# Kernel tuning notes

Hardware: AMD Instinct MI355X
Metric: run time of the kernel (lower is better)

Reference implementation:

```python
import jax, jax.numpy as jnp
import numpy as np

K = 7        # kernel_dim
P = 3        # padding
G = 1        # groups
EPS = 1e-5   # BatchNorm eps


def _unfold(X):
    # X: (B, C, H, W) -> patches (B, C, K*K, H, W), torch.nn.Unfold ordering (C major, then kh, kw)
    B, C, H, W = X.shape
    Xp = jnp.pad(X, ((0, 0), (0, 0), (P, P), (P, P)))
    pats = [Xp[:, :, i:i + H, j:j + W] for i in range(K) for j in range(K)]
    return jnp.stack(pats, axis=2)


def setup_inputs() -> dict:
    key = jax.random.key(0)
    ks = jax.random.split(key, 4)
    B, C, H, W = 2, 64, 128, 128
    Cr = 16  # out_dim // reduction
    return {
        "X": jax.random.normal(ks[0], (B, C, H, W), dtype=jnp.float32),
        "w_reduce": jax.random.normal(ks[1], (Cr, C), dtype=jnp.float32) * 0.05,
        "b_reduce": jnp.zeros((Cr,), dtype=jnp.float32),
        "gamma": jnp.ones((Cr,), dtype=jnp.float32),
        "beta": jnp.zeros((Cr,), dtype=jnp.float32),
        "w_span": jax.random.normal(ks[2], (K * K * G, Cr), dtype=jnp.float32) * 0.05,
        "b_span": jnp.zeros((K * K * G,), dtype=jnp.float32),
    }


def reference(X, w_reduce, b_reduce, gamma, beta, w_span, b_span):
    B, C, H, W = X.shape
    out_dim = C  # in_dim == out_dim -> initial_mapping is Identity

    # unfold (im2col): (B, G, out_dim//G, K*K, H, W)
    unfolded = _unfold(X).reshape(B, G, out_dim // G, K * K, H, W)

    # kernel generation: stride==1 -> pool is Identity
    reduced = jnp.einsum('bchw,oc->bohw', X, w_reduce) + b_reduce[None, :, None, None]
    # BatchNorm2d (training mode: batch statistics) + ReLU
    mean = reduced.mean(axis=(0, 2, 3))
    var = reduced.var(axis=(0, 2, 3))
    bn = (reduced - mean[None, :, None, None]) * jax.lax.rsqrt(var + EPS)[None, :, None, None]
    act = jax.nn.relu(bn * gamma[None, :, None, None] + beta[None, :, None, None])

    kernel = jnp.einsum('bchw,kc->bkhw', act, w_span) + b_span[None, :, None, None]
    kernel = kernel.reshape(B, G, K * K, H, W)[:, :, None]  # (B, G, 1, K*K, H, W)

    out = (kernel * unfolded).sum(axis=3)  # (B, G, out_dim//G, H, W)
    return out.reshape(B, out_dim, H, W)
```

## Files before the change

### kernel.cpp

```cpp
#include <hip/hip_runtime.h>
#include <math.h>

constexpr int B  = 2, C = 64, H = 128, W = 128;
constexpr int Cr = 16;
constexpr int K  = 7, KK = 49;
constexpr int HW  = H * W;
constexpr int CHW = C * HW;
constexpr int NPIX = B * HW;
constexpr float EPS = 1e-5f;

constexpr int R_F = NPIX * Cr;
constexpr int P_F = 512 * 32;
constexpr size_t WS_NEED = (size_t)(R_F + P_F + 64) * 4;

typedef _Float16 half4v __attribute__((ext_vector_type(4)));


__global__ __launch_bounds__(256) void k_reduce_r(
    const float* __restrict__ X, const float* __restrict__ w_reduce,
    const float* __restrict__ b_reduce, float* __restrict__ r_ws,
    float* __restrict__ partial)
{
    __shared__ float wrS[Cr * C];
    __shared__ float tmpA[4][Cr][64];
    const int t = threadIdx.x;
    for (int i = t; i < Cr * C; i += 256) wrS[i] = w_reduce[i];
    __syncthreads();

    const int pixl = t & 63, cg = t >> 6;
    const int p = blockIdx.x * 64 + pixl;
    const int b = p >> 14, hw = p & (HW - 1);
    const float* xb = X + (size_t)b * CHW + hw;

    float x[16];
    #pragma unroll
    for (int i = 0; i < 16; ++i) x[i] = xb[(cg * 16 + i) * HW];

    float rp[16];
    #pragma unroll
    for (int o = 0; o < 16; ++o) rp[o] = (cg == 0) ? b_reduce[o] : 0.f;
    #pragma unroll
    for (int i = 0; i < 16; ++i) {
        const float xv = x[i];
        #pragma unroll
        for (int o = 0; o < 16; ++o)
            rp[o] = fmaf(xv, wrS[o * 64 + cg * 16 + i], rp[o]);
    }
    #pragma unroll
    for (int o = 0; o < 16; ++o) tmpA[cg][o][pixl] = rp[o];
    __syncthreads();

    float rr[4];
    #pragma unroll
    for (int j = 0; j < 4; ++j) {
        const int o = cg * 4 + j;
        rr[j] = tmpA[0][o][pixl] + tmpA[1][o][pixl] + tmpA[2][o][pixl] + tmpA[3][o][pixl];
    }
    *(float4*)&r_ws[(size_t)p * 16 + cg * 4] = make_float4(rr[0], rr[1], rr[2], rr[3]);

    float s[4], q[4];
    #pragma unroll
    for (int j = 0; j < 4; ++j) { s[j] = rr[j]; q[j] = rr[j] * rr[j]; }
    #pragma unroll
    for (int off = 32; off > 0; off >>= 1) {
        #pragma unroll
        for (int j = 0; j < 4; ++j) {
            s[j] += __shfl_down(s[j], off);
            q[j] += __shfl_down(q[j], off);
        }
    }
    if ((t & 63) == 0) {
        #pragma unroll
        for (int j = 0; j < 4; ++j) {
            partial[blockIdx.x * 32 + cg * 4 + j]      = s[j];
            partial[blockIdx.x * 32 + 16 + cg * 4 + j] = q[j];
        }
    }
}

constexpr int TLH = 8, TLW = 16;
constexpr int HR = TLH + 6, HC = TLW + 6;
constexpr int RPT6 = 24;
constexpr int CSP6 = HR * RPT6;

__global__ __launch_bounds__(256) void k_inv6(
    const float* __restrict__ X, const float* __restrict__ r_ws,
    const float* __restrict__ partial, const float* __restrict__ gamma,
    const float* __restrict__ beta, const float* __restrict__ w_span,
    const float* __restrict__ b_span, float* __restrict__ out)
{
    __shared__ _Float16 Xs[32 * CSP6];
    __shared__ _Float16 kcS[KK * 128];
    __shared__ float wspS[KK * Cr];
    __shared__ float bspS[KK + 3];
    __shared__ float red[256];
    __shared__ float scS[16], ofS[16];

    const int t   = threadIdx.x;
    const int raw = blockIdx.x;
    const int wg  = (raw & 7) * 64 + (raw >> 3);
    const int tile = wg & 127;
    const int half = (wg >> 7) & 1;
    const int b    = wg >> 8;
    const int th0 = (tile >> 3) * TLH;
    const int tw0 = (tile & 7) * TLW;

    const int px = t & 127;
    const int kh2 = t >> 7;
    const int p1r = px >> 4, p1c = px & 15;
    const size_t gp = (size_t)b * HW + (size_t)(th0 + p1r) * W + (tw0 + p1c);
    const float4 r0 = *(const float4*)&r_ws[gp * 16 + 0];
    const float4 r1 = *(const float4*)&r_ws[gp * 16 + 4];
    const float4 r2 = *(const float4*)&r_ws[gp * 16 + 8];
    const float4 r3 = *(const float4*)&r_ws[gp * 16 + 12];

    {
        const int scol = t & 31;
        const int sch  = t >> 5;
        const int gw   = tw0 + scol - 3;
        const bool wok = (unsigned)gw < (unsigned)W;
        const float* xg = X + (size_t)b * CHW + (size_t)(half * 32) * HW;
        #pragma unroll
        for (int cb = 0; cb < 4; ++cb) {
            const int c = cb * 8 + sch;
            const float* xc = xg + (size_t)c * HW;
            _Float16* xs = Xs + c * CSP6 + scol;
            #pragma unroll
            for (int r = 0; r < HR; ++r) {
                const int gh = th0 + r - 3;
                float v = 0.f;
                if (wok && (unsigned)gh < (unsigned)H) v = xc[gh * W + gw];
                if (scol < HC) xs[r * RPT6] = (_Float16)v;
            }
        }
    }

    if (t < 196) *(float4*)&wspS[t * 4] = *(const float4*)&w_span[t * 4];
    if (t >= 196 && t < 196 + KK) bspS[t - 196] = b_span[t - 196];

    {
        const int o = t & 31, seg = t >> 5;
        float acc = 0.f;
        #pragma unroll 16
        for (int j = 0; j < 64; ++j) acc += partial[(size_t)(seg * 64 + j) * 32 + o];
        red[seg * 32 + o] = acc;
    }
    __syncthreads();
    if (t < 64) {
        const int o2 = t & 31;
        float tot = 0.f;
        #pragma unroll
        for (int g = 0; g < 8; ++g) tot += red[g * 32 + o2];
        const float sq = __shfl(tot, (t & 31) + 16);
        if (t < 16) {
            const float mean = tot / (float)NPIX;
            const float var  = sq / (float)NPIX - mean * mean;
            const float sc   = gamma[t] * rsqrtf(var + EPS);
            scS[t] = sc;
            ofS[t] = beta[t] - mean * sc;
        }
    }
    __syncthreads();

    {
        float act[16];
        const float rv[16] = {r0.x, r0.y, r0.z, r0.w, r1.x, r1.y, r1.z, r1.w,
                              r2.x, r2.y, r2.z, r2.w, r3.x, r3.y, r3.z, r3.w};
        #pragma unroll
        for (int o = 0; o < 16; ++o)
            act[o] = fmaxf(fmaf(scS[o], rv[o], ofS[o]), 0.f);
        #pragma unroll
        for (int j = 0; j < 25; ++j) {
            const int k = kh2 * 25 + j;
            if (k < KK) {
                const float4 w0 = *(const float4*)&wspS[k * 16 + 0];
                const float4 w1 = *(const float4*)&wspS[k * 16 + 4];
                const float4 w2 = *(const float4*)&wspS[k * 16 + 8];
                const float4 w3 = *(const float4*)&wspS[k * 16 + 12];
                float v = bspS[k];
                v = fmaf(act[0],  w0.x, v); v = fmaf(act[1],  w0.y, v);
                v = fmaf(act[2],  w0.z, v); v = fmaf(act[3],  w0.w, v);
                v = fmaf(act[4],  w1.x, v); v = fmaf(act[5],  w1.y, v);
                v = fmaf(act[6],  w1.z, v); v = fmaf(act[7],  w1.w, v);
                v = fmaf(act[8],  w2.x, v); v = fmaf(act[9],  w2.y, v);
                v = fmaf(act[10], w2.z, v); v = fmaf(act[11], w2.w, v);
                v = fmaf(act[12], w3.x, v); v = fmaf(act[13], w3.y, v);
                v = fmaf(act[14], w3.z, v); v = fmaf(act[15], w3.w, v);
                kcS[k * 128 + px] = (_Float16)v;
            }
        }
    }
    __syncthreads();

    const int strip = t & 31;
    const int chg   = t >> 5;
    const int pr3 = strip >> 2, pc = (strip & 3) * 4;
    const int c0  = chg * 4;

    float acc[4][4];
    #pragma unroll
    for (int i = 0; i < 4; ++i)
        #pragma unroll
        for (int j = 0; j < 4; ++j) acc[i][j] = 0.f;

    #pragma unroll
    for (int kh = 0; kh < 7; ++kh) {
        half4v kcr[7];
        #pragma unroll
        for (int kw = 0; kw < 7; ++kw)
            kcr[kw] = *(const half4v*)&kcS[(kh * 7 + kw) * 128 + pr3 * 16 + pc];
        #pragma unroll
        for (int i = 0; i < 4; ++i) {
            const _Float16* xr = &Xs[(c0 + i) * CSP6 + (pr3 + kh) * RPT6 + pc];
            const half4v xa = *(const half4v*)&xr[0];
            const half4v xb = *(const half4v*)&xr[4];
            const half4v xc = *(const half4v*)&xr[8];
            const _Float16 xw[12] = {xa[0], xa[1], xa[2], xa[3],
                                     xb[0], xb[1], xb[2], xb[3],
                                     xc[0], xc[1], xc[2], xc[3]};
            #pragma unroll
            for (int kw = 0; kw < 7; ++kw)
                #pragma unroll
                for (int j = 0; j < 4; ++j)
                    acc[i][j] = fmaf((float)kcr[kw][j], (float)xw[kw + j], acc[i][j]);
        }
    }

    float* ob = out + (size_t)b * CHW + (size_t)(half * 32 + c0) * HW
                    + (size_t)(th0 + pr3) * W + (tw0 + pc);
    #pragma unroll
    for (int i = 0; i < 4; ++i)
        *(float4*)&ob[(size_t)i * HW] = make_float4(acc[i][0], acc[i][1], acc[i][2], acc[i][3]);
}


constexpr int XS_F  = C * 196;
constexpr int KC_F  = KK * 64;
constexpr int ACT_F = Cr * 64;
constexpr int WR_F  = Cr * C;
constexpr int WSP_F = KK * Cr;
constexpr int SMEM_F = XS_F + KC_F + ACT_F + WR_F + WSP_F + KK + Cr + Cr;
constexpr int SMEM_BYTES = SMEM_F * 4;

__global__ __launch_bounds__(128) void k_reduce_stats(
    const float* __restrict__ X, const float* __restrict__ w_reduce,
    const float* __restrict__ b_reduce, float* __restrict__ partial)
{
    __shared__ float wr[WR_F];
    __shared__ float brd[Cr];
    __shared__ float tmp[2][32];
    const int t = threadIdx.x;
    for (int i = t; i < WR_F; i += 128) wr[i] = w_reduce[i];
    if (t < Cr) brd[t] = b_reduce[t];
    __syncthreads();
    const int p  = blockIdx.x * 128 + t;
    const int b  = p >> 14;
    const int hw = p & (HW - 1);
    const float* xb = X + b * CHW + hw;
    float r[Cr];
    #pragma unroll
    for (int o = 0; o < Cr; ++o) r[o] = brd[o];
    #pragma unroll 4
    for (int c = 0; c < C; ++c) {
        const float x = xb[c * HW];
        #pragma unroll
        for (int o = 0; o < Cr; ++o) r[o] = fmaf(x, wr[o * C + c], r[o]);
    }
    const int lane = t & 63, wv = t >> 6;
    #pragma unroll
    for (int o = 0; o < Cr; ++o) {
        float s = r[o], q = r[o] * r[o];
        #pragma unroll
        for (int off = 32; off > 0; off >>= 1) {
            s += __shfl_down(s, off);
            q += __shfl_down(q, off);
        }
        if (lane == 0) { tmp[wv][o] = s; tmp[wv][Cr + o] = q; }
    }
    __syncthreads();
    if (t < 32) partial[blockIdx.x * 32 + t] = tmp[0][t] + tmp[1][t];
}

__global__ __launch_bounds__(256) void k_stats_final(
    const float* __restrict__ partial, float* __restrict__ stats)
{
    __shared__ float red[256];
    __shared__ float fin[32];
    const int t = threadIdx.x;
    const int o = t & 31, g = t >> 5;
    float acc = 0.f;
    #pragma unroll 8
    for (int j = 0; j < 32; ++j) acc += partial[(g * 32 + j) * 32 + o];
    red[t] = acc;
    __syncthreads();
    if (t < 32) {
        float v = 0.f;
        #pragma unroll
        for (int g2 = 0; g2 < 8; ++g2) v += red[g2 * 32 + t];
        fin[t] = v;
    }
    __syncthreads();
    if (t < Cr) {
        const float mean = fin[t] / (float)NPIX;
        const float var  = fin[Cr + t] / (float)NPIX - mean * mean;
        stats[t]      = mean;
        stats[Cr + t] = rsqrtf(var + EPS);
    }
}

__global__ __launch_bounds__(256) void k_involution(
    const float* __restrict__ X, const float* __restrict__ w_reduce,
    const float* __restrict__ b_reduce, const float* __restrict__ gamma,
    const float* __restrict__ beta, const float* __restrict__ w_span,
    const float* __restrict__ b_span, const float* __restrict__ stats,
    float* __restrict__ out)
{
    extern __shared__ float smem[];
    float* Xs   = smem;
    float* kcS  = Xs  + XS_F;
    float* actS = kcS + KC_F;
    float* wrS  = actS + ACT_F;
    float* wspS = wrS + WR_F;
    float* bspS = wspS + WSP_F;
    float* scS  = bspS + KK;
    float* ofS  = scS + Cr;
    const int t    = threadIdx.x;
    const int bx   = blockIdx.x;
    const int b    = bx >> 8;
    const int tile = bx & 255;
    const int h0   = (tile >> 4) << 3;
    const int w0   = (tile & 15) << 3;
    const float* xbg = X + b * CHW;
    for (int idx = t; idx < XS_F; idx += 256) {
        const int c   = idx / 196;
        const int rem = idx - c * 196;
        const int r   = rem / 14;
        const int col = rem - r * 14;
        const int gh  = h0 + r - 3, gw = w0 + col - 3;
        float v = 0.f;
        if ((unsigned)gh < (unsigned)H && (unsigned)gw < (unsigned)W)
            v = xbg[c * HW + gh * W + gw];
        Xs[idx] = v;
    }
    for (int i = t; i < WR_F;  i += 256) wrS[i]  = w_reduce[i];
    for (int i = t; i < WSP_F; i += 256) wspS[i] = w_span[i];
    if (t < KK) bspS[t] = b_span[t];
    if (t < Cr) {
        const float m  = stats[t];
        const float rs = stats[Cr + t];
        const float gm = gamma[t];
        scS[t] = gm * rs;
        ofS[t] = (b_reduce[t] - m) * gm * rs + beta[t];
    }
    __syncthreads();
    const int pix = t & 63;
    const int grp = t >> 6;
    const int ph  = pix >> 3, pw = pix & 7;
    {
        const int base = (ph + 3) * 14 + (pw + 3);
        float d0 = 0.f, d1 = 0.f, d2 = 0.f, d3 = 0.f;
        #pragma unroll 8
        for (int c = 0; c < C; ++c) {
            const float x = Xs[c * 196 + base];
            d0 = fmaf(x, wrS[(grp * 4 + 0) * C + c], d0);
            d1 = fmaf(x, wrS[(grp * 4 + 1) * C + c], d1);
            d2 = fmaf(x, wrS[(grp * 4 + 2) * C + c], d2);
            d3 = fmaf(x, wrS[(grp * 4 + 3) * C + c], d3);
        }
        const float d[4] = {d0, d1, d2, d3};
        #pragma unroll
        for (int j = 0; j < 4; ++j) {
            const int o = grp * 4 + j;
            actS[o * 64 + pix] = fmaxf(fmaf(scS[o], d[j], ofS[o]), 0.f);
        }
    }
    __syncthreads();
    for (int k = grp; k < KK; k += 4) {
        float v = bspS[k];
        #pragma unroll
        for (int o = 0; o < Cr; ++o)
            v = fmaf(actS[o * 64 + pix], wspS[k * Cr + o], v);
        kcS[k * 64 + pix] = v;
    }
    __syncthreads();
    float acc[16];
    #pragma unroll
    for (int i = 0; i < 16; ++i) acc[i] = 0.f;
    const float* xsc = Xs + grp * 16 * 196;
    #pragma unroll
    for (int k = 0; k < KK; ++k) {
        const int kh = k / 7, kw = k - (k / 7) * 7;
        const float kcv = kcS[k * 64 + pix];
        const int xoff = (ph + kh) * 14 + (pw + kw);
        #pragma unroll
        for (int i = 0; i < 16; ++i)
            acc[i] = fmaf(kcv, xsc[i * 196 + xoff], acc[i]);
    }
    float* ob = out + b * CHW + (grp * 16) * HW + (h0 + ph) * W + (w0 + pw);
    #pragma unroll
    for (int i = 0; i < 16; ++i) ob[i * HW] = acc[i];
}


extern "C" void kernel_launch(void* const* d_in, const int* in_sizes, int n_in,
                              void* d_out, int out_size, void* d_ws, size_t ws_size,
                              hipStream_t stream) {
    const float* X        = (const float*)d_in[0];
    const float* w_reduce = (const float*)d_in[1];
    const float* b_reduce = (const float*)d_in[2];
    const float* gamma    = (const float*)d_in[3];
    const float* beta     = (const float*)d_in[4];
    const float* w_span   = (const float*)d_in[5];
    const float* b_span   = (const float*)d_in[6];
    float* out = (float*)d_out;
    float* ws  = (float*)d_ws;

    if (ws_size >= WS_NEED) {
        float* r_ws    = ws;
        float* partial = ws + R_F;
        k_reduce_r<<<512, 256, 0, stream>>>(X, w_reduce, b_reduce, r_ws, partial);
        k_inv6<<<512, 256, 0, stream>>>(X, r_ws, partial, gamma, beta,
                                        w_span, b_span, out);
    } else {
        float* partial = ws;
        float* stats   = ws + 8192;
        hipFuncSetAttribute((const void*)k_involution,
                            hipFuncAttributeMaxDynamicSharedMemorySize, SMEM_BYTES);
        k_reduce_stats<<<256, 128, 0, stream>>>(X, w_reduce, b_reduce, partial);
        k_stats_final<<<1, 256, 0, stream>>>(partial, stats);
        k_involution<<<512, 256, SMEM_BYTES, stream>>>(
            X, w_reduce, b_reduce, gamma, beta, w_span, b_span, stats, out);
    }
}
```

Baseline: 28.96 us.

## Split reduce kernel across more blocks and transpose BN partial sums layout

The 1x1 reduce kernel now uses 32 pixels per block with 8 channel groups, launching 1024 blocks instead of 512 to expose more parallelism and memory-level concurrency. BatchNorm partial sums are stored transposed (channel-major, 1024 entries each) so the consumer kernel can read them with coalesced float4 loads instead of strided scalar loads. The trade-off is more partials to reduce per block in the main kernel and a larger shared-memory cross-group reduction.

```diff
diff --git a/kernel.cpp b/kernel.cpp
--- a/kernel.cpp
+++ b/kernel.cpp
@@ -9,72 +9,72 @@
 constexpr int NPIX = B * HW;
 constexpr float EPS = 1e-5f;
 
-constexpr int R_F = NPIX * Cr;
-constexpr int P_F = 512 * 32;
-constexpr size_t WS_NEED = (size_t)(R_F + P_F + 64) * 4;
+constexpr int R_F  = NPIX * Cr;
+constexpr int PT_F = 32 * 1024;
+constexpr size_t WS_NEED = (size_t)(R_F + PT_F + 64) * 4;
 
 typedef _Float16 half4v __attribute__((ext_vector_type(4)));
 
 
-__global__ __launch_bounds__(256) void k_reduce_r(
+__global__ __launch_bounds__(256) void k_reduce_r2(
     const float* __restrict__ X, const float* __restrict__ w_reduce,
     const float* __restrict__ b_reduce, float* __restrict__ r_ws,
-    float* __restrict__ partial)
+    float* __restrict__ partialT)
 {
     __shared__ float wrS[Cr * C];
-    __shared__ float tmpA[4][Cr][64];
+    __shared__ float brd[Cr];
+    __shared__ float tmpA[8][Cr][32];
     const int t = threadIdx.x;
-    for (int i = t; i < Cr * C; i += 256) wrS[i] = w_reduce[i];
-    __syncthreads();
-
-    const int pixl = t & 63, cg = t >> 6;
-    const int p = blockIdx.x * 64 + pixl;
+    #pragma unroll
+    for (int i = 0; i < 4; ++i) wrS[t + i * 256] = w_reduce[t + i * 256];
+    if (t < Cr) brd[t] = b_reduce[t];
+    __syncthreads();
+
+    const int pixl = t & 31, cg = t >> 5;
+    const int p = blockIdx.x * 32 + pixl;
     const int b = p >> 14, hw = p & (HW - 1);
     const float* xb = X + (size_t)b * CHW + hw;
 
-    float x[16];
-    #pragma unroll
-    for (int i = 0; i < 16; ++i) x[i] = xb[(cg * 16 + i) * HW];
+    float x[8];
+    #pragma unroll
+    for (int i = 0; i < 8; ++i) x[i] = xb[(cg * 8 + i) * HW];
 
     float rp[16];
     #pragma unroll
-    for (int o = 0; o < 16; ++o) rp[o] = (cg == 0) ? b_reduce[o] : 0.f;
-    #pragma unroll
-    for (int i = 0; i < 16; ++i) {
+    for (int o = 0; o < 16; ++o) rp[o] = 0.f;
+    #pragma unroll
+    for (int i = 0; i < 8; ++i) {
         const float xv = x[i];
         #pragma unroll
         for (int o = 0; o < 16; ++o)
-            rp[o] = fmaf(xv, wrS[o * 64 + cg * 16 + i], rp[o]);
+            rp[o] = fmaf(xv, wrS[o * 64 + cg * 8 + i], rp[o]);
     }
     #pragma unroll
     for (int o = 0; o < 16; ++o) tmpA[cg][o][pixl] = rp[o];
     __syncthreads();
 
-    float rr[4];
-    #pragma unroll
-    for (int j = 0; j < 4; ++j) {
-        const int o = cg * 4 + j;
-        rr[j] = tmpA[0][o][pixl] + tmpA[1][o][pixl] + tmpA[2][o][pixl] + tmpA[3][o][pixl];
-    }
-    *(float4*)&r_ws[(size_t)p * 16 + cg * 4] = make_float4(rr[0], rr[1], rr[2], rr[3]);
-
-    float s[4], q[4];
-    #pragma unroll
-    for (int j = 0; j < 4; ++j) { s[j] = rr[j]; q[j] = rr[j] * rr[j]; }
-    #pragma unroll
-    for (int off = 32; off > 0; off >>= 1) {
-        #pragma unroll
-        for (int j = 0; j < 4; ++j) {
-            s[j] += __shfl_down(s[j], off);
-            q[j] += __shfl_down(q[j], off);
-        }
-    }
-    if ((t & 63) == 0) {
-        #pragma unroll
-        for (int j = 0; j < 4; ++j) {
-            partial[blockIdx.x * 32 + cg * 4 + j]      = s[j];
-            partial[blockIdx.x * 32 + 16 + cg * 4 + j] = q[j];
-        }
+    const int o0 = cg * 2;
+    float r0 = brd[o0], r1 = brd[o0 + 1];
+    #pragma unroll
+    for (int g = 0; g < 8; ++g) {
+        r0 += tmpA[g][o0][pixl];
+        r1 += tmpA[g][o0 + 1][pixl];
+    }
+    *(float2*)&r_ws[(size_t)p * 16 + o0] = make_float2(r0, r1);
+
+    float s0 = r0, q0 = r0 * r0, s1 = r1, q1 = r1 * r1;
+    #pragma unroll
+    for (int off = 16; off > 0; off >>= 1) {
+        s0 += __shfl_down(s0, off);
+        q0 += __shfl_down(q0, off);
+        s1 += __shfl_down(s1, off);
+        q1 += __shfl_down(q1, off);
+    }
+    if (pixl == 0) {
+        partialT[(size_t)o0 * 1024 + blockIdx.x]            = s0;
+        partialT[(size_t)(o0 + 1) * 1024 + blockIdx.x]      = s1;
+        partialT[(size_t)(16 + o0) * 1024 + blockIdx.x]     = q0;
+        partialT[(size_t)(16 + o0 + 1) * 1024 + blockIdx.x] = q1;
     }
 }
 
@@ -85,7 +85,7 @@
 
 __global__ __launch_bounds__(256) void k_inv6(
     const float* __restrict__ X, const float* __restrict__ r_ws,
-    const float* __restrict__ partial, const float* __restrict__ gamma,
+    const float* __restrict__ partialT, const float* __restrict__ gamma,
     const float* __restrict__ beta, const float* __restrict__ w_span,
     const float* __restrict__ b_span, float* __restrict__ out)
 {
@@ -140,9 +140,13 @@
 
     {
         const int o = t & 31, seg = t >> 5;
+        const float4* pp = (const float4*)&partialT[(size_t)o * 1024 + seg * 128];
         float acc = 0.f;
-        #pragma unroll 16
-        for (int j = 0; j < 64; ++j) acc += partial[(size_t)(seg * 64 + j) * 32 + o];
+        #pragma unroll 8
+        for (int j = 0; j < 32; ++j) {
+            const float4 v = pp[j];
+            acc += v.x + v.y + v.z + v.w;
+        }
         red[seg * 32 + o] = acc;
     }
     __syncthreads();
@@ -416,10 +420,10 @@
     float* ws  = (float*)d_ws;
 
     if (ws_size >= WS_NEED) {
-        float* r_ws    = ws;
-        float* partial = ws + R_F;
-        k_reduce_r<<<512, 256, 0, stream>>>(X, w_reduce, b_reduce, r_ws, partial);
-        k_inv6<<<512, 256, 0, stream>>>(X, r_ws, partial, gamma, beta,
+        float* r_ws     = ws;
+        float* partialT = ws + R_F;
+        k_reduce_r2<<<1024, 256, 0, stream>>>(X, w_reduce, b_reduce, r_ws, partialT);
+        k_inv6<<<512, 256, 0, stream>>>(X, r_ws, partialT, gamma, beta,
                                         w_span, b_span, out);
     } else {
         float* partial = ws;
```

Result: slower. 34.38 us (+18.7%).
